# Performance work log

Hardware: AMD Instinct MI355X
Metric: run time of the kernel (lower is better)

## Reference

```python
import jax, jax.numpy as jnp
import numpy as np

N, T, IN_DIM = 5000, 100, 32
FEAT, HID, OUT, HEADS = 64, 64, 8, 4
E = 160000
F_IN = FEAT + OUT  # GATCell input = concat(embedding, theta)


def setup_inputs() -> dict:
    key = jax.random.key(0)
    ks = jax.random.split(key, 16)
    s = 0.05
    d = {}
    d["x"] = jax.random.normal(ks[0], (N, T, IN_DIM), jnp.float32)
    d["edge_index"] = jax.random.randint(ks[1], (2, E), 0, N, dtype=jnp.int32)
    # LSTM params (PyTorch gate order: i, f, g, o)
    d["W_ih"] = jax.random.normal(ks[2], (IN_DIM, 4 * FEAT), jnp.float32) * s
    d["W_hh"] = jax.random.normal(ks[3], (FEAT, 4 * FEAT), jnp.float32) * s
    d["b_ih"] = jax.random.normal(ks[4], (4 * FEAT,), jnp.float32) * s
    d["b_hh"] = jax.random.normal(ks[5], (4 * FEAT,), jnp.float32) * s
    # TransformerConv params (lin_q/k/v with bias, lin_skip with bias; concat=False)
    d["Wq"] = jax.random.normal(ks[6], (F_IN, HEADS * HID), jnp.float32) * s
    d["bq"] = jax.random.normal(ks[7], (HEADS * HID,), jnp.float32) * s
    d["Wk"] = jax.random.normal(ks[8], (F_IN, HEADS * HID), jnp.float32) * s
    d["bk"] = jax.random.normal(ks[9], (HEADS * HID,), jnp.float32) * s
    d["Wv"] = jax.random.normal(ks[10], (F_IN, HEADS * HID), jnp.float32) * s
    d["bv"] = jax.random.normal(ks[11], (HEADS * HID,), jnp.float32) * s
    d["Wskip"] = jax.random.normal(ks[12], (F_IN, HID), jnp.float32) * s
    d["bskip"] = jax.random.normal(ks[13], (HID,), jnp.float32) * s
    # GATCell mlp (bias=False)
    d["Wmlp"] = jax.random.normal(ks[14], (HID, OUT), jnp.float32) * s
    return d


def _lstm(x, W_ih, W_hh, b_ih, b_hh):
    # x: [N, T, IN_DIM] -> embedding [T, N, FEAT]
    xs = jnp.transpose(x, (1, 0, 2))

    def step(carry, xt):
        h, c = carry
        gates = xt @ W_ih + h @ W_hh + (b_ih + b_hh)
        i, f, g, o = jnp.split(gates, 4, axis=-1)
        c = jax.nn.sigmoid(f) * c + jax.nn.sigmoid(i) * jnp.tanh(g)
        h = jax.nn.sigmoid(o) * jnp.tanh(c)
        return (h, c), h

    h0 = jnp.zeros((x.shape[0], FEAT), x.dtype)
    _, hs = jax.lax.scan(step, (h0, h0), xs)
    return hs


def _transformer_conv(h, edge_index, Wq, bq, Wk, bk, Wv, bv, Wskip, bskip):
    # h: [N, F_IN]; edge_index: [2, E] (row 0 = source j, row 1 = target i)
    n = h.shape[0]
    src, dst = edge_index[0], edge_index[1]
    q = (h @ Wq + bq).reshape(n, HEADS, HID)
    k = (h @ Wk + bk).reshape(n, HEADS, HID)
    v = (h @ Wv + bv).reshape(n, HEADS, HID)
    # per-edge attention logits [E, HEADS]
    alpha = jnp.einsum('ehd,ehd->eh', q[dst], k[src]) / jnp.sqrt(jnp.float32(HID))
    # segment softmax over incoming edges of each target node
    m = jax.ops.segment_max(alpha, dst, num_segments=n)
    m = jnp.where(jnp.isfinite(m), m, 0.0)
    ex = jnp.exp(alpha - m[dst])
    denom = jax.ops.segment_sum(ex, dst, num_segments=n)
    w = ex / jnp.maximum(denom[dst], 1e-16)
    agg = jax.ops.segment_sum(w[:, :, None] * v[src], dst, num_segments=n)  # [N,H,D]
    out = agg.mean(axis=1)  # concat=False -> average heads
    return out + h @ Wskip + bskip  # root skip connection


def reference(x, edge_index, W_ih, W_hh, b_ih, b_hh, Wq, bq, Wk, bk, Wv, bv,
              Wskip, bskip, Wmlp):
    emb = _lstm(x, W_ih, W_hh, b_ih, b_hh)  # [T, N, FEAT]
    n = x.shape[0]

    def gat_step(theta, emb_t):
        h_in = jnp.concatenate([emb_t, theta], axis=-1)  # [N, F_IN]
        hid = _transformer_conv(h_in, edge_index, Wq, bq, Wk, bk, Wv, bv,
                                Wskip, bskip)
        theta_new = jnp.tanh(hid) @ Wmlp
        return theta_new, theta_new

    theta0 = jnp.zeros((n, OUT), x.dtype)
    _, thetas = jax.lax.scan(gat_step, theta0, emb)  # [T, N, OUT]
    theta = jnp.transpose(thetas, (1, 0, 2))  # [N, T, OUT]

    alpha_beta = theta[:, :, :-3]
    a_b = jax.nn.sigmoid(theta[:, :, -3:-1])
    a = a_b[:, :, 0:1] * a_b[:, :, 1:]
    b = a_b[:, :, 0:1] - a
    c = jax.nn.softplus(theta[:, :, -1:])
    return jnp.concatenate([alpha_beta, a, b, c], axis=-1)
```

## Files before the change

kernel.cpp:

```cpp
#include <hip/hip_runtime.h>
#include <math.h>

#define NN 5000
#define TT 100
#define IND 32
#define FEATD 64
#define HIDD 64
#define OUTD 8
#define NHEADS 4
#define EE 160000
#define FIN 72
#define NHC 256
#define QKV_B 625
#define LSTM_B 625

typedef float floatx2 __attribute__((ext_vector_type(2)));

__device__ __forceinline__ float fsig(float x){ return 1.f/(1.f+__expf(-x)); }
__device__ __forceinline__ float ftanh(float x){ return 1.f - 2.f/(__expf(2.f*x)+1.f); }
__device__ __forceinline__ float fsoftplus(float x){ return (x>20.f)? x : log1pf(__expf(x)); }

__global__ __launch_bounds__(256) void count_edges(const int* __restrict__ dst,
                                                   int* __restrict__ cnt){
    int e = blockIdx.x*256 + threadIdx.x;
    if (e < EE) atomicAdd(&cnt[dst[e]], 1);
}

#define SCAN_N 5120
__global__ __launch_bounds__(1024) void scan_csr(const int* __restrict__ cnt,
                                                 int* __restrict__ row_ptr,
                                                 int* __restrict__ cursor){
    __shared__ int sa[SCAN_N];
    __shared__ int sb[SCAN_N];
    int tid = threadIdx.x;
    for (int i=tid;i<SCAN_N;i+=1024) sa[i] = (i<NN)?cnt[i]:0;
    __syncthreads();
    int *s=sa, *d=sb;
    for (int off=1; off<SCAN_N; off<<=1){
        for (int i=tid;i<SCAN_N;i+=1024){
            int v = s[i];
            if (i>=off) v += s[i-off];
            d[i] = v;
        }
        __syncthreads();
        int* t=s; s=d; d=t;
    }
    for (int i=tid;i<=NN;i+=1024){
        int excl = (i==0)?0:s[i-1];
        row_ptr[i] = excl;
        if (i<NN) cursor[i] = excl;
    }
}

__global__ __launch_bounds__(256) void fill_edges(const int* __restrict__ src,
                                                  const int* __restrict__ dst,
                                                  int* __restrict__ cursor,
                                                  int* __restrict__ col){
    int e = blockIdx.x*256 + threadIdx.x;
    if (e < EE){
        int dn = dst[e];
        int pos = atomicAdd(&cursor[dn], 1);
        col[pos] = src[e];
    }
}

#define LOADKV(e) (*reinterpret_cast<const uint2*>(kv + (size_t)col[(e)]*512 + lane*8))
__global__ __launch_bounds__(256) void attn_step(
    const float* __restrict__ q,
    const unsigned char* __restrict__ kv,
    const float* __restrict__ sk,
    const int* __restrict__ row_ptr,
    const int* __restrict__ col,
    const float* __restrict__ Wmlp,
    float* __restrict__ theta,
    float* __restrict__ out,
    int ts)
{
    __shared__ float mrg[2][5][64];
    int tid = threadIdx.x;
    int wvid = tid >> 6;
    int lane = tid & 63;
    int ln   = wvid >> 1;
    int half = wvid & 1;
    int n = blockIdx.x*2 + ln;
    int e0 = row_ptr[n], e1 = row_ptr[n+1];
    float4 qv = *reinterpret_cast<const float4*>(q + n*NHC + lane*4);
    qv.x *= 0.125f; qv.y *= 0.125f; qv.z *= 0.125f; qv.w *= 0.125f;

    float denA=0.f, denB=0.f;
    float aA0=0.f, aA1=0.f, aA2=0.f, aA3=0.f;
    float aB0=0.f, aB1=0.f, aB2=0.f, aB3=0.f;

    const uint2 zv = {0u,0u};
    uint2 bA0=zv, bA1=zv, bB0=zv, bB1=zv;
    int base = e0 + half;
    if (base     < e1) bA0 = LOADKV(base);
    if (base + 2 < e1) bB0 = LOADKV(base+2);
    if (base + 4 < e1) bA1 = LOADKV(base+4);
    if (base + 6 < e1) bB1 = LOADKV(base+6);
    for (int e = base; e < e1; e += 4){
        uint2 uA = bA0; bA0 = bA1; bA1 = zv;
        uint2 uB = bB0; bB0 = bB1; bB1 = zv;
        if (e + 8  < e1) bA1 = LOADKV(e+8);
        if (e + 10 < e1) bB1 = LOADKV(e+10);

        floatx2 kA0 = __builtin_amdgcn_cvt_pk_f32_fp8(uA.x, false);
        floatx2 kA1 = __builtin_amdgcn_cvt_pk_f32_fp8(uA.x, true);
        floatx2 kB0 = __builtin_amdgcn_cvt_pk_f32_fp8(uB.x, false);
        floatx2 kB1 = __builtin_amdgcn_cvt_pk_f32_fp8(uB.x, true);
        float pA = qv.x*kA0[0] + qv.y*kA0[1] + qv.z*kA1[0] + qv.w*kA1[1];
        float pB = qv.x*kB0[0] + qv.y*kB0[1] + qv.z*kB1[0] + qv.w*kB1[1];
        pA += __shfl_xor(pA,1); pB += __shfl_xor(pB,1);
        pA += __shfl_xor(pA,2); pB += __shfl_xor(pB,2);
        pA += __shfl_xor(pA,4); pB += __shfl_xor(pB,4);
        pA += __shfl_xor(pA,8); pB += __shfl_xor(pB,8);

        float eA = __expf(pA);
        float eB = __expf((e + 2 < e1) ? pB : -INFINITY);
        floatx2 vA0 = __builtin_amdgcn_cvt_pk_f32_fp8(uA.y, false);
        floatx2 vA1 = __builtin_amdgcn_cvt_pk_f32_fp8(uA.y, true);
        floatx2 vB0 = __builtin_amdgcn_cvt_pk_f32_fp8(uB.y, false);
        floatx2 vB1 = __builtin_amdgcn_cvt_pk_f32_fp8(uB.y, true);
        denA += eA;
        aA0 = fmaf(eA, vA0[0], aA0);
        aA1 = fmaf(eA, vA0[1], aA1);
        aA2 = fmaf(eA, vA1[0], aA2);
        aA3 = fmaf(eA, vA1[1], aA3);
        denB += eB;
        aB0 = fmaf(eB, vB0[0], aB0);
        aB1 = fmaf(eB, vB0[1], aB1);
        aB2 = fmaf(eB, vB1[0], aB2);
        aB3 = fmaf(eB, vB1[1], aB3);
    }
    float denom = denA + denB;
    float ax = aA0 + aB0;
    float ay = aA1 + aB1;
    float az = aA2 + aB2;
    float aw = aA3 + aB3;

    if (half == 1){
        mrg[ln][0][lane]=denom;
        mrg[ln][1][lane]=ax; mrg[ln][2][lane]=ay;
        mrg[ln][3][lane]=az; mrg[ln][4][lane]=aw;
    }
    __syncthreads();
    if (half == 1) return;

    denom += mrg[ln][0][lane];
    ax += mrg[ln][1][lane];
    ay += mrg[ln][2][lane];
    az += mrg[ln][3][lane];
    aw += mrg[ln][4][lane];

    float inv = 1.f / fmaxf(denom, 1e-16f);
    ax *= inv; ay *= inv; az *= inv; aw *= inv;
    ax += __shfl_xor(ax,16); ax += __shfl_xor(ax,32);
    ay += __shfl_xor(ay,16); ay += __shfl_xor(ay,32);
    az += __shfl_xor(az,16); az += __shfl_xor(az,32);
    aw += __shfl_xor(aw,16); aw += __shfl_xor(aw,32);
    int d0 = (lane & 15) * 4;
    float4 skv = *reinterpret_cast<const float4*>(sk + n*64 + d0);
    float t0 = ftanh(0.25f*ax + skv.x);
    float t1 = ftanh(0.25f*ay + skv.y);
    float t2 = ftanh(0.25f*az + skv.z);
    float t3 = ftanh(0.25f*aw + skv.w);
    float p8[8];
    #pragma unroll
    for (int j=0;j<8;j++){
        p8[j] = fmaf(t0, Wmlp[(d0+0)*8+j],
                fmaf(t1, Wmlp[(d0+1)*8+j],
                fmaf(t2, Wmlp[(d0+2)*8+j],
                     t3* Wmlp[(d0+3)*8+j])));
    }
    #pragma unroll
    for (int j=0;j<8;j++){
        p8[j] += __shfl_xor(p8[j],1);
        p8[j] += __shfl_xor(p8[j],2);
        p8[j] += __shfl_xor(p8[j],4);
        p8[j] += __shfl_xor(p8[j],8);
    }
    if (lane == 0){
        float4 t0v = {p8[0],p8[1],p8[2],p8[3]};
        float4 t1v = {p8[4],p8[5],p8[6],p8[7]};
        *reinterpret_cast<float4*>(theta + n*8)     = t0v;
        *reinterpret_cast<float4*>(theta + n*8 + 4) = t1v;
        float ab0 = fsig(p8[5]);
        float ab1 = fsig(p8[6]);
        float a  = ab0*ab1;
        float bb = ab0 - a;
        float cc = fsoftplus(p8[7]);
        float4 o0 = {p8[0],p8[1],p8[2],p8[3]};
        float4 o1 = {p8[4],a,bb,cc};
        float* op = out + ((size_t)n*TT + ts)*8;
        *reinterpret_cast<float4*>(op)     = o0;
        *reinterpret_cast<float4*>(op + 4) = o1;
    }
}

__global__ __launch_bounds__(256) void qkv_lstm_step(
    const float* __restrict__ x,
    const float* __restrict__ W_ih, const float* __restrict__ W_hh,
    const float* __restrict__ b_ih, const float* __restrict__ b_hh,
    float* __restrict__ h0, float* __restrict__ h1,
    float* __restrict__ c,
    const float* __restrict__ theta,
    const float* __restrict__ Wq, const float* __restrict__ bq,
    const float* __restrict__ Wk, const float* __restrict__ bk,
    const float* __restrict__ Wv, const float* __restrict__ bv,
    const float* __restrict__ Wsk, const float* __restrict__ bsk,
    float* __restrict__ q, float* __restrict__ sk,
    unsigned char* __restrict__ kv, int t)
{
    int tid = threadIdx.x;
    if (blockIdx.x < QKV_B){
        if (t < 0) return;
        __shared__ float hin[8][72];
        const float* hread = (t & 1) ? h1 : h0;
        int n0 = blockIdx.x * 8;
        for (int i=tid; i<8*72; i+=256){
            int node = i/72, kk = i%72;
            int n = n0 + node;
            hin[node][kk] = (kk<64) ? hread[n*64+kk] : theta[n*8 + (kk-64)];
        }
        __syncthreads();

        if (tid < 208){
            int c4 = tid*4;
            const float* W; const float* b; int ncol; int cc; int kind;
            if (c4 < 256)      { W=Wq;  b=bq;  ncol=256; cc=c4;     kind=0; }
            else if (c4 < 512) { W=Wk;  b=bk;  ncol=256; cc=c4-256; kind=1; }
            else if (c4 < 768) { W=Wv;  b=bv;  ncol=256; cc=c4-512; kind=2; }
            else               { W=Wsk; b=bsk; ncol=64;  cc=c4-768; kind=3; }
            float acc2[8][4];
            #pragma unroll
            for (int nn=0;nn<8;nn++){
                #pragma unroll
                for (int j=0;j<4;j++) acc2[nn][j]=0.f;
            }
            #pragma unroll 4
            for (int kk=0; kk<FIN; kk++){
                float4 w = *reinterpret_cast<const float4*>(W + kk*ncol + cc);
                #pragma unroll
                for (int nn=0;nn<8;nn++){
                    float xv = hin[nn][kk];
                    acc2[nn][0]=fmaf(xv,w.x,acc2[nn][0]);
                    acc2[nn][1]=fmaf(xv,w.y,acc2[nn][1]);
                    acc2[nn][2]=fmaf(xv,w.z,acc2[nn][2]);
                    acc2[nn][3]=fmaf(xv,w.w,acc2[nn][3]);
                }
            }
            float4 bb = *reinterpret_cast<const float4*>(b + cc);
            #pragma unroll
            for (int nn=0;nn<8;nn++){
                int n = n0 + nn;
                float o0=acc2[nn][0]+bb.x, o1=acc2[nn][1]+bb.y;
                float o2=acc2[nn][2]+bb.z, o3=acc2[nn][3]+bb.w;
                if (kind == 0){
                    float4 o = {o0,o1,o2,o3};
                    *reinterpret_cast<float4*>(q + n*NHC + cc) = o;
                } else if (kind == 3){
                    float4 o = {o0,o1,o2,o3};
                    *reinterpret_cast<float4*>(sk + n*64 + cc) = o;
                } else {
                    int pk = __builtin_amdgcn_cvt_pk_fp8_f32(o0, o1, 0,  false);
                    pk     = __builtin_amdgcn_cvt_pk_fp8_f32(o2, o3, pk, true);
                    int off = n*512 + cc*2 + ((kind==2)?4:0);
                    *reinterpret_cast<unsigned int*>(kv + off) = (unsigned int)pk;
                }
            }
        }
    } else {
        int s = t + 1;
        if (s >= TT) return;
        __shared__ float xh[8][96];
        const float* hread = (s & 1) ? h0 : h1;
        float*       hwrit = (s & 1) ? h1 : h0;
        int n0 = (blockIdx.x - QKV_B) * 8;
        for (int i=tid; i<8*96; i+=256){
            int node = i/96, kk = i%96;
            int n = n0 + node;
            xh[node][kk] = (kk<32) ? x[(n*TT + s)*IND + kk] : hread[n*64 + (kk-32)];
        }
        __syncthreads();

        int d  = tid & 63;
        int wv = tid >> 6;
        float acc[2][4];
        #pragma unroll
        for (int p=0;p<2;p++){
            #pragma unroll
            for (int g=0;g<4;g++) acc[p][g]=0.f;
        }
        #pragma unroll 8
        for (int kk=0; kk<32; kk++){
            const float* Wr = W_ih + kk*256;
            float w0=Wr[d], w1=Wr[d+64], w2=Wr[d+128], w3=Wr[d+192];
            float x0 = xh[wv][kk], x1 = xh[wv+4][kk];
            acc[0][0]=fmaf(x0,w0,acc[0][0]); acc[0][1]=fmaf(x0,w1,acc[0][1]);
            acc[0][2]=fmaf(x0,w2,acc[0][2]); acc[0][3]=fmaf(x0,w3,acc[0][3]);
            acc[1][0]=fmaf(x1,w0,acc[1][0]); acc[1][1]=fmaf(x1,w1,acc[1][1]);
            acc[1][2]=fmaf(x1,w2,acc[1][2]); acc[1][3]=fmaf(x1,w3,acc[1][3]);
        }
        #pragma unroll 8
        for (int kk=0; kk<64; kk++){
            const float* Wr = W_hh + kk*256;
            float w0=Wr[d], w1=Wr[d+64], w2=Wr[d+128], w3=Wr[d+192];
            float x0 = xh[wv][32+kk], x1 = xh[wv+4][32+kk];
            acc[0][0]=fmaf(x0,w0,acc[0][0]); acc[0][1]=fmaf(x0,w1,acc[0][1]);
            acc[0][2]=fmaf(x0,w2,acc[0][2]); acc[0][3]=fmaf(x0,w3,acc[0][3]);
            acc[1][0]=fmaf(x1,w0,acc[1][0]); acc[1][1]=fmaf(x1,w1,acc[1][1]);
            acc[1][2]=fmaf(x1,w2,acc[1][2]); acc[1][3]=fmaf(x1,w3,acc[1][3]);
        }
        float bi0 = b_ih[d]     + b_hh[d];
        float bi1 = b_ih[d+64]  + b_hh[d+64];
        float bi2 = b_ih[d+128] + b_hh[d+128];
        float bi3 = b_ih[d+192] + b_hh[d+192];
        #pragma unroll
        for (int p=0;p<2;p++){
            int n = n0 + wv + p*4;
            float gi = fsig (acc[p][0] + bi0);
            float gf = fsig (acc[p][1] + bi1);
            float gg = ftanh(acc[p][2] + bi2);
            float go = fsig (acc[p][3] + bi3);
            float cold = c[n*64 + d];
            float cnew = gf*cold + gi*gg;
            float hnew = go*ftanh(cnew);
            c[n*64 + d] = cnew;
            hwrit[n*64 + d] = hnew;
        }
    }
}

extern "C" void kernel_launch(void* const* d_in, const int* in_sizes, int n_in,
                              void* d_out, int out_size, void* d_ws, size_t ws_size,
                              hipStream_t stream) {
    const float* x     = (const float*)d_in[0];
    const int*   ei    = (const int*)  d_in[1];
    const float* W_ih  = (const float*)d_in[2];
    const float* W_hh  = (const float*)d_in[3];
    const float* b_ih  = (const float*)d_in[4];
    const float* b_hh  = (const float*)d_in[5];
    const float* Wq    = (const float*)d_in[6];
    const float* bq    = (const float*)d_in[7];
    const float* Wk    = (const float*)d_in[8];
    const float* bk    = (const float*)d_in[9];
    const float* Wv    = (const float*)d_in[10];
    const float* bv    = (const float*)d_in[11];
    const float* Wsk   = (const float*)d_in[12];
    const float* bsk   = (const float*)d_in[13];
    const float* Wmlp  = (const float*)d_in[14];
    float* out = (float*)d_out;

    float* f = (float*)d_ws;
    float* h0    = f;
    float* h1    = h0 + NN*64;
    float* c     = h1 + NN*64;
    float* theta = c + NN*64;
    float* q     = theta + NN*8;
    float* skb   = q + NN*NHC;
    unsigned char* kvb = (unsigned char*)(skb + NN*64);
    int* ip      = (int*)(kvb + (size_t)NN*512);
    int* row_ptr = ip;
    int* cnt     = row_ptr + (NN+1);
    int* cursor  = cnt + NN;
    int* colv    = cursor + NN;

    const int* src = ei;
    const int* dst = ei + EE;

    hipMemsetAsync(h0, 0, (size_t)NN*(64+64+64+8)*sizeof(float), stream);
    hipMemsetAsync(cnt, 0, (size_t)NN*sizeof(int), stream);

    count_edges<<<(EE+255)/256, 256, 0, stream>>>(dst, cnt);
    scan_csr<<<1, 1024, 0, stream>>>(cnt, row_ptr, cursor);
    fill_edges<<<(EE+255)/256, 256, 0, stream>>>(src, dst, cursor, colv);

    qkv_lstm_step<<<QKV_B + LSTM_B, 256, 0, stream>>>(
        x, W_ih, W_hh, b_ih, b_hh, h0, h1, c, theta,
        Wq,bq, Wk,bk, Wv,bv, Wsk,bsk, q, skb, kvb, -1);

    for (int t=0; t<TT; t++){
        if (t >= 1)
            attn_step<<<NN/2, 256, 0, stream>>>(q, kvb, skb, row_ptr, colv,
                                                Wmlp, theta, out, t-1);
        qkv_lstm_step<<<QKV_B + LSTM_B, 256, 0, stream>>>(
            x, W_ih, W_hh, b_ih, b_hh, h0, h1, c, theta,
            Wq,bq, Wk,bk, Wv,bv, Wsk,bsk, q, skb, kvb, t);
    }
    attn_step<<<NN/2, 256, 0, stream>>>(q, kvb, skb, row_ptr, colv,
                                        Wmlp, theta, out, TT-1);
}
```

Measured before the change: 5.073 ms.

## Fuse attention step with QKV projection into one per-timestep kernel

Merges the per-timestep attention kernel and the QKV/skip projection into a single launch. Each attention block now feeds its freshly computed theta straight from shared memory into the projection of its own two nodes, and the LSTM blocks run alongside in the same launch. The K/V fp8 buffer is double-buffered so neighbours' keys can be read while new ones are written, and the separate theta buffer and initial memset are removed. This halves the number of kernel launches and serialization points per step, but the projection now covers only two nodes per block instead of eight, so each block rereads the weights over fewer nodes and total weight traffic rises.

```diff
diff --git a/kernel.cpp b/kernel.cpp
--- a/kernel.cpp
+++ b/kernel.cpp
@@ -11,7 +11,7 @@
 #define EE 160000
 #define FIN 72
 #define NHC 256
-#define QKV_B 625
+#define ATTN_B 2500
 #define LSTM_B 625
 
 typedef float floatx2 __attribute__((ext_vector_type(2)));
@@ -64,17 +64,273 @@
     }
 }
 
-#define LOADKV(e) (*reinterpret_cast<const uint2*>(kv + (size_t)col[(e)]*512 + lane*8))
-__global__ __launch_bounds__(256) void attn_step(
+#define LOADKV(e) (*reinterpret_cast<const uint2*>(kvr + (size_t)col[(e)]*512 + lane*8))
+__global__ __launch_bounds__(256) void step_kernel(
+    const float* __restrict__ x,
+    const float* __restrict__ W_ih, const float* __restrict__ W_hh,
+    const float* __restrict__ b_ih, const float* __restrict__ b_hh,
+    float* __restrict__ h0, float* __restrict__ h1,
+    float* __restrict__ c,
+    const float* __restrict__ Wq, const float* __restrict__ bq,
+    const float* __restrict__ Wk, const float* __restrict__ bk,
+    const float* __restrict__ Wv, const float* __restrict__ bv,
+    const float* __restrict__ Wsk, const float* __restrict__ bsk,
+    float* __restrict__ q, float* __restrict__ sk,
+    const unsigned char* __restrict__ kvr,
+    unsigned char* __restrict__ kvw,
+    const int* __restrict__ row_ptr,
+    const int* __restrict__ col,
+    const float* __restrict__ Wmlp,
+    float* __restrict__ out,
+    int t)
+{
+    int tid = threadIdx.x;
+    if (blockIdx.x < ATTN_B){
+        if (t < 0) return;
+        __shared__ float mrg[2][5][64];
+        __shared__ float hin[2][FIN];
+        int wvid = tid >> 6;
+        int lane = tid & 63;
+        int ln   = wvid >> 1;
+        int half = wvid & 1;
+        int n = blockIdx.x*2 + ln;
+
+        const float* hread = (t & 1) ? h1 : h0;
+        for (int i=tid; i<2*64; i+=256){
+            int node = i>>6, kk = i&63;
+            hin[node][kk] = hread[(blockIdx.x*2+node)*64 + kk];
+        }
+        if (t == 0){
+            if (tid < 16){ int node=tid>>3, j=tid&7; hin[node][64+j] = 0.f; }
+        }
+
+        float denom, ax, ay, az, aw;
+        if (t >= 1){
+            int e0 = row_ptr[n], e1 = row_ptr[n+1];
+            float4 qv = *reinterpret_cast<const float4*>(q + n*NHC + lane*4);
+            qv.x *= 0.125f; qv.y *= 0.125f; qv.z *= 0.125f; qv.w *= 0.125f;
+
+            float denA=0.f, denB=0.f;
+            float aA0=0.f, aA1=0.f, aA2=0.f, aA3=0.f;
+            float aB0=0.f, aB1=0.f, aB2=0.f, aB3=0.f;
+            const uint2 zv = {0u,0u};
+            uint2 bA0=zv, bA1=zv, bB0=zv, bB1=zv;
+            int base = e0 + half;
+            if (base     < e1) bA0 = LOADKV(base);
+            if (base + 2 < e1) bB0 = LOADKV(base+2);
+            if (base + 4 < e1) bA1 = LOADKV(base+4);
+            if (base + 6 < e1) bB1 = LOADKV(base+6);
+            for (int e = base; e < e1; e += 4){
+                uint2 uA = bA0; bA0 = bA1; bA1 = zv;
+                uint2 uB = bB0; bB0 = bB1; bB1 = zv;
+                if (e + 8  < e1) bA1 = LOADKV(e+8);
+                if (e + 10 < e1) bB1 = LOADKV(e+10);
+
+                floatx2 kA0 = __builtin_amdgcn_cvt_pk_f32_fp8(uA.x, false);
+                floatx2 kA1 = __builtin_amdgcn_cvt_pk_f32_fp8(uA.x, true);
+                floatx2 kB0 = __builtin_amdgcn_cvt_pk_f32_fp8(uB.x, false);
+                floatx2 kB1 = __builtin_amdgcn_cvt_pk_f32_fp8(uB.x, true);
+                float pA = qv.x*kA0[0] + qv.y*kA0[1] + qv.z*kA1[0] + qv.w*kA1[1];
+                float pB = qv.x*kB0[0] + qv.y*kB0[1] + qv.z*kB1[0] + qv.w*kB1[1];
+                pA += __shfl_xor(pA,1); pB += __shfl_xor(pB,1);
+                pA += __shfl_xor(pA,2); pB += __shfl_xor(pB,2);
+                pA += __shfl_xor(pA,4); pB += __shfl_xor(pB,4);
+                pA += __shfl_xor(pA,8); pB += __shfl_xor(pB,8);
+
+                float eA = __expf(pA);
+                float eB = __expf((e + 2 < e1) ? pB : -INFINITY);
+                floatx2 vA0 = __builtin_amdgcn_cvt_pk_f32_fp8(uA.y, false);
+                floatx2 vA1 = __builtin_amdgcn_cvt_pk_f32_fp8(uA.y, true);
+                floatx2 vB0 = __builtin_amdgcn_cvt_pk_f32_fp8(uB.y, false);
+                floatx2 vB1 = __builtin_amdgcn_cvt_pk_f32_fp8(uB.y, true);
+                denA += eA;
+                aA0 = fmaf(eA, vA0[0], aA0);
+                aA1 = fmaf(eA, vA0[1], aA1);
+                aA2 = fmaf(eA, vA1[0], aA2);
+                aA3 = fmaf(eA, vA1[1], aA3);
+                denB += eB;
+                aB0 = fmaf(eB, vB0[0], aB0);
+                aB1 = fmaf(eB, vB0[1], aB1);
+                aB2 = fmaf(eB, vB1[0], aB2);
+                aB3 = fmaf(eB, vB1[1], aB3);
+            }
+            denom = denA + denB;
+            ax = aA0 + aB0; ay = aA1 + aB1;
+            az = aA2 + aB2; aw = aA3 + aB3;
+            if (half == 1){
+                mrg[ln][0][lane]=denom;
+                mrg[ln][1][lane]=ax; mrg[ln][2][lane]=ay;
+                mrg[ln][3][lane]=az; mrg[ln][4][lane]=aw;
+            }
+        }
+        __syncthreads();
+        if (t >= 1 && half == 0){
+            denom += mrg[ln][0][lane];
+            ax += mrg[ln][1][lane];
+            ay += mrg[ln][2][lane];
+            az += mrg[ln][3][lane];
+            aw += mrg[ln][4][lane];
+            float inv = 1.f / fmaxf(denom, 1e-16f);
+            ax *= inv; ay *= inv; az *= inv; aw *= inv;
+            ax += __shfl_xor(ax,16); ax += __shfl_xor(ax,32);
+            ay += __shfl_xor(ay,16); ay += __shfl_xor(ay,32);
+            az += __shfl_xor(az,16); az += __shfl_xor(az,32);
+            aw += __shfl_xor(aw,16); aw += __shfl_xor(aw,32);
+            int d0 = (lane & 15) * 4;
+            float4 skv = *reinterpret_cast<const float4*>(sk + n*64 + d0);
+            float t0 = ftanh(0.25f*ax + skv.x);
+            float t1 = ftanh(0.25f*ay + skv.y);
+            float t2 = ftanh(0.25f*az + skv.z);
+            float t3 = ftanh(0.25f*aw + skv.w);
+            float p8[8];
+            #pragma unroll
+            for (int j=0;j<8;j++){
+                p8[j] = fmaf(t0, Wmlp[(d0+0)*8+j],
+                        fmaf(t1, Wmlp[(d0+1)*8+j],
+                        fmaf(t2, Wmlp[(d0+2)*8+j],
+                             t3* Wmlp[(d0+3)*8+j])));
+            }
+            #pragma unroll
+            for (int j=0;j<8;j++){
+                p8[j] += __shfl_xor(p8[j],1);
+                p8[j] += __shfl_xor(p8[j],2);
+                p8[j] += __shfl_xor(p8[j],4);
+                p8[j] += __shfl_xor(p8[j],8);
+            }
+            if (lane == 0){
+                #pragma unroll
+                for (int j=0;j<8;j++) hin[ln][64+j] = p8[j];
+                float ab0 = fsig(p8[5]);
+                float ab1 = fsig(p8[6]);
+                float a  = ab0*ab1;
+                float bb = ab0 - a;
+                float cc = fsoftplus(p8[7]);
+                float4 o0 = {p8[0],p8[1],p8[2],p8[3]};
+                float4 o1 = {p8[4],a,bb,cc};
+                float* op = out + ((size_t)n*TT + (t-1))*8;
+                *reinterpret_cast<float4*>(op)     = o0;
+                *reinterpret_cast<float4*>(op + 4) = o1;
+            }
+        }
+        __syncthreads();
+
+        if (tid < 208){
+            int c4 = tid*4;
+            const float* W; const float* b; int ncol; int cc; int kind;
+            if (c4 < 256)      { W=Wq;  b=bq;  ncol=256; cc=c4;     kind=0; }
+            else if (c4 < 512) { W=Wk;  b=bk;  ncol=256; cc=c4-256; kind=1; }
+            else if (c4 < 768) { W=Wv;  b=bv;  ncol=256; cc=c4-512; kind=2; }
+            else               { W=Wsk; b=bsk; ncol=64;  cc=c4-768; kind=3; }
+            float acc2[2][4];
+            #pragma unroll
+            for (int nn=0;nn<2;nn++){
+                #pragma unroll
+                for (int j=0;j<4;j++) acc2[nn][j]=0.f;
+            }
+            #pragma unroll 4
+            for (int kk=0; kk<FIN; kk++){
+                float4 w = *reinterpret_cast<const float4*>(W + kk*ncol + cc);
+                #pragma unroll
+                for (int nn=0;nn<2;nn++){
+                    float xv = hin[nn][kk];
+                    acc2[nn][0]=fmaf(xv,w.x,acc2[nn][0]);
+                    acc2[nn][1]=fmaf(xv,w.y,acc2[nn][1]);
+                    acc2[nn][2]=fmaf(xv,w.z,acc2[nn][2]);
+                    acc2[nn][3]=fmaf(xv,w.w,acc2[nn][3]);
+                }
+            }
+            float4 bb = *reinterpret_cast<const float4*>(b + cc);
+            #pragma unroll
+            for (int nn=0;nn<2;nn++){
+                int n2 = blockIdx.x*2 + nn;
+                float o0=acc2[nn][0]+bb.x, o1=acc2[nn][1]+bb.y;
+                float o2=acc2[nn][2]+bb.z, o3=acc2[nn][3]+bb.w;
+                if (kind == 0){
+                    float4 o = {o0,o1,o2,o3};
+                    *reinterpret_cast<float4*>(q + n2*NHC + cc) = o;
+                } else if (kind == 3){
+                    float4 o = {o0,o1,o2,o3};
+                    *reinterpret_cast<float4*>(sk + n2*64 + cc) = o;
+                } else {
+                    int pk = __builtin_amdgcn_cvt_pk_fp8_f32(o0, o1, 0,  false);
+                    pk     = __builtin_amdgcn_cvt_pk_fp8_f32(o2, o3, pk, true);
+                    int off = n2*512 + cc*2 + ((kind==2)?4:0);
+                    *reinterpret_cast<unsigned int*>(kvw + off) = (unsigned int)pk;
+                }
+            }
+        }
+    } else {
+        int s = t + 1;
+        if (s >= TT) return;
+        __shared__ float xh[8][96];
+        const float* hread = (s & 1) ? h0 : h1;
+        float*       hwrit = (s & 1) ? h1 : h0;
+        int n0 = (blockIdx.x - ATTN_B) * 8;
+        for (int i=tid; i<8*96; i+=256){
+            int node = i/96, kk = i%96;
+            int n = n0 + node;
+            xh[node][kk] = (kk<32) ? x[(n*TT + s)*IND + kk]
+                                   : ((s == 0) ? 0.f : hread[n*64 + (kk-32)]);
+        }
+        __syncthreads();
+
+        int d  = tid & 63;
+        int wv = tid >> 6;
+        float acc[2][4];
+        #pragma unroll
+        for (int p=0;p<2;p++){
+            #pragma unroll
+            for (int g=0;g<4;g++) acc[p][g]=0.f;
+        }
+        #pragma unroll 8
+        for (int kk=0; kk<32; kk++){
+            const float* Wr = W_ih + kk*256;
+            float w0=Wr[d], w1=Wr[d+64], w2=Wr[d+128], w3=Wr[d+192];
+            float x0 = xh[wv][kk], x1 = xh[wv+4][kk];
+            acc[0][0]=fmaf(x0,w0,acc[0][0]); acc[0][1]=fmaf(x0,w1,acc[0][1]);
+            acc[0][2]=fmaf(x0,w2,acc[0][2]); acc[0][3]=fmaf(x0,w3,acc[0][3]);
+            acc[1][0]=fmaf(x1,w0,acc[1][0]); acc[1][1]=fmaf(x1,w1,acc[1][1]);
+            acc[1][2]=fmaf(x1,w2,acc[1][2]); acc[1][3]=fmaf(x1,w3,acc[1][3]);
+        }
+        #pragma unroll 8
+        for (int kk=0; kk<64; kk++){
+            const float* Wr = W_hh + kk*256;
+            float w0=Wr[d], w1=Wr[d+64], w2=Wr[d+128], w3=Wr[d+192];
+            float x0 = xh[wv][32+kk], x1 = xh[wv+4][32+kk];
+            acc[0][0]=fmaf(x0,w0,acc[0][0]); acc[0][1]=fmaf(x0,w1,acc[0][1]);
+            acc[0][2]=fmaf(x0,w2,acc[0][2]); acc[0][3]=fmaf(x0,w3,acc[0][3]);
+            acc[1][0]=fmaf(x1,w0,acc[1][0]); acc[1][1]=fmaf(x1,w1,acc[1][1]);
+            acc[1][2]=fmaf(x1,w2,acc[1][2]); acc[1][3]=fmaf(x1,w3,acc[1][3]);
+        }
+        float bi0 = b_ih[d]     + b_hh[d];
+        float bi1 = b_ih[d+64]  + b_hh[d+64];
+        float bi2 = b_ih[d+128] + b_hh[d+128];
+        float bi3 = b_ih[d+192] + b_hh[d+192];
+        #pragma unroll
+        for (int p=0;p<2;p++){
+            int n = n0 + wv + p*4;
+            float gi = fsig (acc[p][0] + bi0);
+            float gf = fsig (acc[p][1] + bi1);
+            float gg = ftanh(acc[p][2] + bi2);
+            float go = fsig (acc[p][3] + bi3);
+            float cold = (s == 0) ? 0.f : c[n*64 + d];
+            float cnew = gf*cold + gi*gg;
+            float hnew = go*ftanh(cnew);
+            c[n*64 + d] = cnew;
+            hwrit[n*64 + d] = hnew;
+        }
+    }
+}
+
+#define LOADKV2(e) (*reinterpret_cast<const uint2*>(kv + (size_t)col[(e)]*512 + lane*8))
+__global__ __launch_bounds__(256) void attn_final(
     const float* __restrict__ q,
     const unsigned char* __restrict__ kv,
     const float* __restrict__ sk,
     const int* __restrict__ row_ptr,
     const int* __restrict__ col,
     const float* __restrict__ Wmlp,
-    float* __restrict__ theta,
-    float* __restrict__ out,
-    int ts)
+    float* __restrict__ out)
 {
     __shared__ float mrg[2][5][64];
     int tid = threadIdx.x;
@@ -90,20 +346,18 @@
     float denA=0.f, denB=0.f;
     float aA0=0.f, aA1=0.f, aA2=0.f, aA3=0.f;
     float aB0=0.f, aB1=0.f, aB2=0.f, aB3=0.f;
-
     const uint2 zv = {0u,0u};
     uint2 bA0=zv, bA1=zv, bB0=zv, bB1=zv;
     int base = e0 + half;
-    if (base     < e1) bA0 = LOADKV(base);
-    if (base + 2 < e1) bB0 = LOADKV(base+2);
-    if (base + 4 < e1) bA1 = LOADKV(base+4);
-    if (base + 6 < e1) bB1 = LOADKV(base+6);
+    if (base     < e1) bA0 = LOADKV2(base);
+    if (base + 2 < e1) bB0 = LOADKV2(base+2);
+    if (base + 4 < e1) bA1 = LOADKV2(base+4);
+    if (base + 6 < e1) bB1 = LOADKV2(base+6);
     for (int e = base; e < e1; e += 4){
         uint2 uA = bA0; bA0 = bA1; bA1 = zv;
         uint2 uB = bB0; bB0 = bB1; bB1 = zv;
-        if (e + 8  < e1) bA1 = LOADKV(e+8);
-        if (e + 10 < e1) bB1 = LOADKV(e+10);
-
+        if (e + 8  < e1) bA1 = LOADKV2(e+8);
+        if (e + 10 < e1) bB1 = LOADKV2(e+10);
         floatx2 kA0 = __builtin_amdgcn_cvt_pk_f32_fp8(uA.x, false);
         floatx2 kA1 = __builtin_amdgcn_cvt_pk_f32_fp8(uA.x, true);
         floatx2 kB0 = __builtin_amdgcn_cvt_pk_f32_fp8(uB.x, false);
@@ -114,7 +368,6 @@
         pA += __shfl_xor(pA,2); pB += __shfl_xor(pB,2);
         pA += __shfl_xor(pA,4); pB += __shfl_xor(pB,4);
         pA += __shfl_xor(pA,8); pB += __shfl_xor(pB,8);
-
         float eA = __expf(pA);
         float eB = __expf((e + 2 < e1) ? pB : -INFINITY);
         floatx2 vA0 = __builtin_amdgcn_cvt_pk_f32_fp8(uA.y, false);
@@ -137,7 +390,6 @@
     float ay = aA1 + aB1;
     float az = aA2 + aB2;
     float aw = aA3 + aB3;
-
     if (half == 1){
         mrg[ln][0][lane]=denom;
         mrg[ln][1][lane]=ax; mrg[ln][2][lane]=ay;
@@ -145,13 +397,11 @@
     }
     __syncthreads();
     if (half == 1) return;
-
     denom += mrg[ln][0][lane];
     ax += mrg[ln][1][lane];
     ay += mrg[ln][2][lane];
     az += mrg[ln][3][lane];
     aw += mrg[ln][4][lane];
-
     float inv = 1.f / fmaxf(denom, 1e-16f);
     ax *= inv; ay *= inv; az *= inv; aw *= inv;
     ax += __shfl_xor(ax,16); ax += __shfl_xor(ax,32);
@@ -180,10 +430,6 @@
         p8[j] += __shfl_xor(p8[j],8);
     }
     if (lane == 0){
-        float4 t0v = {p8[0],p8[1],p8[2],p8[3]};
-        float4 t1v = {p8[4],p8[5],p8[6],p8[7]};
-        *reinterpret_cast<float4*>(theta + n*8)     = t0v;
-        *reinterpret_cast<float4*>(theta + n*8 + 4) = t1v;
         float ab0 = fsig(p8[5]);
         float ab1 = fsig(p8[6]);
         float a  = ab0*ab1;
@@ -191,143 +437,9 @@
         float cc = fsoftplus(p8[7]);
         float4 o0 = {p8[0],p8[1],p8[2],p8[3]};
         float4 o1 = {p8[4],a,bb,cc};
-        float* op = out + ((size_t)n*TT + ts)*8;
+        float* op = out + ((size_t)n*TT + (TT-1))*8;
         *reinterpret_cast<float4*>(op)     = o0;
         *reinterpret_cast<float4*>(op + 4) = o1;
-    }
-}
-
-__global__ __launch_bounds__(256) void qkv_lstm_step(
-    const float* __restrict__ x,
-    const float* __restrict__ W_ih, const float* __restrict__ W_hh,
-    const float* __restrict__ b_ih, const float* __restrict__ b_hh,
-    float* __restrict__ h0, float* __restrict__ h1,
-    float* __restrict__ c,
-    const float* __restrict__ theta,
-    const float* __restrict__ Wq, const float* __restrict__ bq,
-    const float* __restrict__ Wk, const float* __restrict__ bk,
-    const float* __restrict__ Wv, const float* __restrict__ bv,
-    const float* __restrict__ Wsk, const float* __restrict__ bsk,
-    float* __restrict__ q, float* __restrict__ sk,
-    unsigned char* __restrict__ kv, int t)
-{
-    int tid = threadIdx.x;
-    if (blockIdx.x < QKV_B){
-        if (t < 0) return;
-        __shared__ float hin[8][72];
-        const float* hread = (t & 1) ? h1 : h0;
-        int n0 = blockIdx.x * 8;
-        for (int i=tid; i<8*72; i+=256){
-            int node = i/72, kk = i%72;
-            int n = n0 + node;
-            hin[node][kk] = (kk<64) ? hread[n*64+kk] : theta[n*8 + (kk-64)];
-        }
-        __syncthreads();
-
-        if (tid < 208){
-            int c4 = tid*4;
-            const float* W; const float* b; int ncol; int cc; int kind;
-            if (c4 < 256)      { W=Wq;  b=bq;  ncol=256; cc=c4;     kind=0; }
-            else if (c4 < 512) { W=Wk;  b=bk;  ncol=256; cc=c4-256; kind=1; }
-            else if (c4 < 768) { W=Wv;  b=bv;  ncol=256; cc=c4-512; kind=2; }
-            else               { W=Wsk; b=bsk; ncol=64;  cc=c4-768; kind=3; }
-            float acc2[8][4];
-            #pragma unroll
-            for (int nn=0;nn<8;nn++){
-                #pragma unroll
-                for (int j=0;j<4;j++) acc2[nn][j]=0.f;
-            }
-            #pragma unroll 4
-            for (int kk=0; kk<FIN; kk++){
-                float4 w = *reinterpret_cast<const float4*>(W + kk*ncol + cc);
-                #pragma unroll
-                for (int nn=0;nn<8;nn++){
-                    float xv = hin[nn][kk];
-                    acc2[nn][0]=fmaf(xv,w.x,acc2[nn][0]);
-                    acc2[nn][1]=fmaf(xv,w.y,acc2[nn][1]);
-                    acc2[nn][2]=fmaf(xv,w.z,acc2[nn][2]);
-                    acc2[nn][3]=fmaf(xv,w.w,acc2[nn][3]);
-                }
-            }
-            float4 bb = *reinterpret_cast<const float4*>(b + cc);
-            #pragma unroll
-            for (int nn=0;nn<8;nn++){
-                int n = n0 + nn;
-                float o0=acc2[nn][0]+bb.x, o1=acc2[nn][1]+bb.y;
-                float o2=acc2[nn][2]+bb.z, o3=acc2[nn][3]+bb.w;
-                if (kind == 0){
-                    float4 o = {o0,o1,o2,o3};
-                    *reinterpret_cast<float4*>(q + n*NHC + cc) = o;
-                } else if (kind == 3){
-                    float4 o = {o0,o1,o2,o3};
-                    *reinterpret_cast<float4*>(sk + n*64 + cc) = o;
-                } else {
-                    int pk = __builtin_amdgcn_cvt_pk_fp8_f32(o0, o1, 0,  false);
-                    pk     = __builtin_amdgcn_cvt_pk_fp8_f32(o2, o3, pk, true);
-                    int off = n*512 + cc*2 + ((kind==2)?4:0);
-                    *reinterpret_cast<unsigned int*>(kv + off) = (unsigned int)pk;
-                }
-            }
-        }
-    } else {
-        int s = t + 1;
-        if (s >= TT) return;
-        __shared__ float xh[8][96];
-        const float* hread = (s & 1) ? h0 : h1;
-        float*       hwrit = (s & 1) ? h1 : h0;
-        int n0 = (blockIdx.x - QKV_B) * 8;
-        for (int i=tid; i<8*96; i+=256){
-            int node = i/96, kk = i%96;
-            int n = n0 + node;
-            xh[node][kk] = (kk<32) ? x[(n*TT + s)*IND + kk] : hread[n*64 + (kk-32)];
-        }
-        __syncthreads();
-
-        int d  = tid & 63;
-        int wv = tid >> 6;
-        float acc[2][4];
-        #pragma unroll
-        for (int p=0;p<2;p++){
-            #pragma unroll
-            for (int g=0;g<4;g++) acc[p][g]=0.f;
-        }
-        #pragma unroll 8
-        for (int kk=0; kk<32; kk++){
-            const float* Wr = W_ih + kk*256;
-            float w0=Wr[d], w1=Wr[d+64], w2=Wr[d+128], w3=Wr[d+192];
-            float x0 = xh[wv][kk], x1 = xh[wv+4][kk];
-            acc[0][0]=fmaf(x0,w0,acc[0][0]); acc[0][1]=fmaf(x0,w1,acc[0][1]);
-            acc[0][2]=fmaf(x0,w2,acc[0][2]); acc[0][3]=fmaf(x0,w3,acc[0][3]);
-            acc[1][0]=fmaf(x1,w0,acc[1][0]); acc[1][1]=fmaf(x1,w1,acc[1][1]);
-            acc[1][2]=fmaf(x1,w2,acc[1][2]); acc[1][3]=fmaf(x1,w3,acc[1][3]);
-        }
-        #pragma unroll 8
-        for (int kk=0; kk<64; kk++){
-            const float* Wr = W_hh + kk*256;
-            float w0=Wr[d], w1=Wr[d+64], w2=Wr[d+128], w3=Wr[d+192];
-            float x0 = xh[wv][32+kk], x1 = xh[wv+4][32+kk];
-            acc[0][0]=fmaf(x0,w0,acc[0][0]); acc[0][1]=fmaf(x0,w1,acc[0][1]);
-            acc[0][2]=fmaf(x0,w2,acc[0][2]); acc[0][3]=fmaf(x0,w3,acc[0][3]);
-            acc[1][0]=fmaf(x1,w0,acc[1][0]); acc[1][1]=fmaf(x1,w1,acc[1][1]);
-            acc[1][2]=fmaf(x1,w2,acc[1][2]); acc[1][3]=fmaf(x1,w3,acc[1][3]);
-        }
-        float bi0 = b_ih[d]     + b_hh[d];
-        float bi1 = b_ih[d+64]  + b_hh[d+64];
-        float bi2 = b_ih[d+128] + b_hh[d+128];
-        float bi3 = b_ih[d+192] + b_hh[d+192];
-        #pragma unroll
-        for (int p=0;p<2;p++){
-            int n = n0 + wv + p*4;
-            float gi = fsig (acc[p][0] + bi0);
-            float gf = fsig (acc[p][1] + bi1);
-            float gg = ftanh(acc[p][2] + bi2);
-            float go = fsig (acc[p][3] + bi3);
-            float cold = c[n*64 + d];
-            float cnew = gf*cold + gi*gg;
-            float hnew = go*ftanh(cnew);
-            c[n*64 + d] = cnew;
-            hwrit[n*64 + d] = hnew;
-        }
     }
 }
 
@@ -355,11 +467,11 @@
     float* h0    = f;
     float* h1    = h0 + NN*64;
     float* c     = h1 + NN*64;
-    float* theta = c + NN*64;
-    float* q     = theta + NN*8;
+    float* q     = c + NN*64;
     float* skb   = q + NN*NHC;
-    unsigned char* kvb = (unsigned char*)(skb + NN*64);
-    int* ip      = (int*)(kvb + (size_t)NN*512);
+    unsigned char* kvb0 = (unsigned char*)(skb + NN*64);
+    unsigned char* kvb1 = kvb0 + (size_t)NN*512;
+    int* ip      = (int*)(kvb1 + (size_t)NN*512);
     int* row_ptr = ip;
     int* cnt     = row_ptr + (NN+1);
     int* cursor  = cnt + NN;
@@ -368,25 +480,20 @@
     const int* src = ei;
     const int* dst = ei + EE;
 
-    hipMemsetAsync(h0, 0, (size_t)NN*(64+64+64+8)*sizeof(float), stream);
     hipMemsetAsync(cnt, 0, (size_t)NN*sizeof(int), stream);
 
     count_edges<<<(EE+255)/256, 256, 0, stream>>>(dst, cnt);
     scan_csr<<<1, 1024, 0, stream>>>(cnt, row_ptr, cursor);
     fill_edges<<<(EE+255)/256, 256, 0, stream>>>(src, dst, cursor, colv);
 
-    qkv_lstm_step<<<QKV_B + LSTM_B, 256, 0, stream>>>(
-        x, W_ih, W_hh, b_ih, b_hh, h0, h1, c, theta,
-        Wq,bq, Wk,bk, Wv,bv, Wsk,bsk, q, skb, kvb, -1);
-
-    for (int t=0; t<TT; t++){
-        if (t >= 1)
-            attn_step<<<NN/2, 256, 0, stream>>>(q, kvb, skb, row_ptr, colv,
-                                                Wmlp, theta, out, t-1);
-        qkv_lstm_step<<<QKV_B + LSTM_B, 256, 0, stream>>>(
-            x, W_ih, W_hh, b_ih, b_hh, h0, h1, c, theta,
-            Wq,bq, Wk,bk, Wv,bv, Wsk,bsk, q, skb, kvb, t);
-    }
-    attn_step<<<NN/2, 256, 0, stream>>>(q, kvb, skb, row_ptr, colv,
-                                        Wmlp, theta, out, TT-1);
-}
+    for (int t=-1; t<TT; t++){
+        const unsigned char* kvr = ((t-1) & 1) ? kvb1 : kvb0;
+        unsigned char*       kvw = (t & 1) ? kvb1 : kvb0;
+        step_kernel<<<ATTN_B + LSTM_B, 256, 0, stream>>>(
+            x, W_ih, W_hh, b_ih, b_hh, h0, h1, c,
+            Wq,bq, Wk,bk, Wv,bv, Wsk,bsk,
+            q, skb, kvr, kvw, row_ptr, colv, Wmlp, out, t);
+    }
+    attn_final<<<NN/2, 256, 0, stream>>>(q, ((TT-1)&1)?kvb1:kvb0, skb,
+                                         row_ptr, colv, Wmlp, out);
+}
```

Result: faster. 4.910 ms (-3.2%).
